# Optimization experiments

Hardware: AMD Instinct MI355X
Metric: run time of the kernel (lower is better)

The kernel has to match this reference:

```python
import jax, jax.numpy as jnp
import numpy as np

B, L, D, H, FF = 2, 4096, 512, 8, 2048
HD = D // H
EPS = 1e-5


def _layer_norm(x, g, b):
    mu = jnp.mean(x, axis=-1, keepdims=True)
    var = jnp.mean(jnp.square(x - mu), axis=-1, keepdims=True)
    return (x - mu) * jax.lax.rsqrt(var + EPS) * g + b


def setup_inputs() -> dict:
    key = jax.random.key(0)
    ks = jax.random.split(key, 16)
    s = 1.0 / np.sqrt(D)
    inp = {
        'x': jax.random.normal(ks[0], (B, L, D), dtype=jnp.float32),
        'Wq': jax.random.normal(ks[1], (D, D), dtype=jnp.float32) * s,
        'bq': jnp.zeros((D,), jnp.float32),
        'Wk': jax.random.normal(ks[2], (D, D), dtype=jnp.float32) * s,
        'bk': jnp.zeros((D,), jnp.float32),
        'Wv': jax.random.normal(ks[3], (D, D), dtype=jnp.float32) * s,
        'bv': jnp.zeros((D,), jnp.float32),
        'Wo': jax.random.normal(ks[4], (D, D), dtype=jnp.float32) * s,
        'bo': jnp.zeros((D,), jnp.float32),
        'ln1_g': jnp.ones((D,), jnp.float32),
        'ln1_b': jnp.zeros((D,), jnp.float32),
        'W1': jax.random.normal(ks[5], (D, FF), dtype=jnp.float32) * s,
        'b1': jnp.zeros((FF,), jnp.float32),
        'W2': jax.random.normal(ks[6], (FF, D), dtype=jnp.float32) * (1.0 / np.sqrt(FF)),
        'b2': jnp.zeros((D,), jnp.float32),
        'ln2_g': jnp.ones((D,), jnp.float32),
        'ln2_b': jnp.zeros((D,), jnp.float32),
        'window': 128,
    }
    return inp


def reference(x, Wq, bq, Wk, bk, Wv, bv, Wo, bo, ln1_g, ln1_b, W1, b1, W2, b2, ln2_g, ln2_b, window):
    # ---- local (banded) self-attention, matching nn.MultiheadAttention math ----
    q = (x @ Wq + bq).reshape(B, L, H, HD)
    k = (x @ Wk + bk).reshape(B, L, H, HD)
    v = (x @ Wv + bv).reshape(B, L, H, HD)
    scale = 1.0 / np.sqrt(HD)
    scores = jnp.einsum('bqhd,bkhd->bhqk', q, k) * scale  # [B,H,L,L]
    idx = jnp.arange(L)
    band = jnp.abs(idx[None, :] - idx[:, None]) > window   # True = masked
    scores = jnp.where(band[None, None], -jnp.inf, scores)
    probs = jax.nn.softmax(scores, axis=-1)
    attn = jnp.einsum('bhqk,bkhd->bqhd', probs, v).reshape(B, L, D)
    attn = attn @ Wo + bo
    # ---- residual + norm1 ----
    h = _layer_norm(x + attn, ln1_g, ln1_b)
    # ---- FFN + residual + norm2 (dropout=0 at eval) ----
    ff = jax.nn.relu(h @ W1 + b1) @ W2 + b2
    return _layer_norm(h + ff, ln2_g, ln2_b)
```

## Files before the change

kernel.cpp:

```cpp
#include <hip/hip_runtime.h>

namespace {

constexpr int B = 2, L = 4096, D = 512, H = 8, FF = 2048;
constexpr int M = B * L;
constexpr float LN_EPS = 1e-5f;

typedef __attribute__((ext_vector_type(8))) short short8;
typedef __attribute__((ext_vector_type(4))) float floatx4;

typedef __attribute__((address_space(3))) unsigned int lds_uint;
typedef const __attribute__((address_space(1))) unsigned int glob_uint;

__device__ __forceinline__ void gl_lds16(const unsigned short* g, unsigned short* l) {
  __builtin_amdgcn_global_load_lds((glob_uint*)g, (lds_uint*)l, 16, 0, 0);
}

__device__ __forceinline__ unsigned short f2bf(float f) {
  union { float f; unsigned u; } v; v.f = f;
  unsigned r = v.u + 0x7FFFu + ((v.u >> 16) & 1u);
  return (unsigned short)(r >> 16);
}

__device__ __forceinline__ float bf2f(unsigned short b) {
  union { unsigned u; float f; } v; v.u = ((unsigned)b) << 16;
  return v.f;
}

__global__ __launch_bounds__(256)
void k_prep(const float* __restrict__ x,
            const float* __restrict__ Wq, const float* __restrict__ Wk,
            const float* __restrict__ Wv, const float* __restrict__ Wo,
            const float* __restrict__ W1, const float* __restrict__ W2,
            const float* __restrict__ bq, const float* __restrict__ bk,
            const float* __restrict__ bv,
            unsigned short* __restrict__ Xb,
            unsigned short* __restrict__ WqkvT, unsigned short* __restrict__ WoT,
            unsigned short* __restrict__ W1T, unsigned short* __restrict__ W2T,
            float* __restrict__ bqkv) {
  __shared__ unsigned short tile[64 * 72];
  if (blockIdx.x < 4102) {
    int tid = blockIdx.x * blockDim.x + threadIdx.x;
    if (tid < 1048576) {
      float4 v = ((const float4*)x)[tid];
      ((ushort4*)Xb)[tid] = make_ushort4(f2bf(v.x), f2bf(v.y), f2bf(v.z), f2bf(v.w));
      return;
    }
    int u = tid - 1048576;
    if (u < 1536) bqkv[u] = (u < 512) ? bq[u] : (u < 1024 ? bk[u - 512] : bv[u - 1024]);
    return;
  }
  const int t = blockIdx.x - 4102;
  const float* src; unsigned short* dst; int Ns, Kd, n0, k0, nsrc0;
  if (t < 192) {
    int nt = t % 24, kt = t / 24; int ng = nt * 64;
    src = ng < 512 ? Wq : (ng < 1024 ? Wk : Wv);
    Ns = 512; Kd = 512; n0 = ng; nsrc0 = ng & 511; k0 = kt * 64; dst = WqkvT;
  } else if (t < 256) {
    int u = t - 192; int nt = u % 8, kt = u / 8;
    src = Wo; Ns = 512; Kd = 512; n0 = nt * 64; nsrc0 = n0; k0 = kt * 64; dst = WoT;
  } else if (t < 512) {
    int u = t - 256; int nt = u % 32, kt = u / 32;
    src = W1; Ns = 2048; Kd = 512; n0 = nt * 64; nsrc0 = n0; k0 = kt * 64; dst = W1T;
  } else {
    int u = t - 512; int nt = u % 8, kt = u / 8;
    src = W2; Ns = 512; Kd = 2048; n0 = nt * 64; nsrc0 = n0; k0 = kt * 64; dst = W2T;
  }
  const int tid = threadIdx.x;
  {
    int r = tid >> 2, cs = (tid & 3) * 16;
    const float4* sp = (const float4*)(src + (size_t)(k0 + r) * Ns + nsrc0 + cs);
    unsigned short* tp = &tile[r * 72 + cs];
#pragma unroll
    for (int i = 0; i < 4; ++i) {
      float4 v = sp[i];
      tp[i * 4 + 0] = f2bf(v.x); tp[i * 4 + 1] = f2bf(v.y);
      tp[i * 4 + 2] = f2bf(v.z); tp[i * 4 + 3] = f2bf(v.w);
    }
  }
  __syncthreads();
  {
    int n = tid >> 2, ks = (tid & 3) * 16;
    unsigned short buf[16];
#pragma unroll
    for (int e = 0; e < 16; ++e) buf[e] = tile[(ks + e) * 72 + n];
    unsigned short* dp = dst + (size_t)(n0 + n) * Kd + k0 + ks;
    *(short8*)dp = *(const short8*)&buf[0];
    *(short8*)(dp + 8) = *(const short8*)&buf[8];
  }
}

template <int EPI>
__global__ __launch_bounds__(256, 3)
void k_gemm(const unsigned short* __restrict__ A, const unsigned short* __restrict__ BT,
            const float* __restrict__ bias, void* __restrict__ Cout,
            unsigned short* __restrict__ Vout,
            const int klen, const int N) {
  __shared__ unsigned short lA[2][128 * 32];
  __shared__ unsigned short lB[2][128 * 32];
  unsigned flat = blockIdx.x + gridDim.x * (blockIdx.y + gridDim.y * blockIdx.z);
  const unsigned chunk = (gridDim.x * gridDim.y * gridDim.z) >> 3;
  flat = (flat & 7) * chunk + (flat >> 3);
  const unsigned bx = flat % gridDim.x;
  const unsigned rest = flat / gridDim.x;
  const unsigned by = rest % gridDim.y;
  const unsigned bz = rest / gridDim.y;

  const int tid = threadIdx.x;
  const int wave = tid >> 6, lane = tid & 63;
  const int quad = lane >> 4, l16 = lane & 15;
  const int m0 = by * 128, n0 = bx * 128;
  const int wm = (wave >> 1) * 64, wn = (wave & 1) * 64;
  const int kbeg = bz * klen;
  const size_t Kdim = (size_t)klen * gridDim.z;

  const floatx4 fzero = {0.f, 0.f, 0.f, 0.f};
  floatx4 acc[4][4];
#pragma unroll
  for (int i = 0; i < 4; ++i)
#pragma unroll
    for (int j = 0; j < 4; ++j) acc[i][j] = fzero;

  const int r0 = tid >> 2, o0 = (tid & 3) * 8;
  const int r1 = (256 + tid) >> 2, o1 = (tid & 3) * 8;
  const unsigned short* Ag0 = A + (size_t)(m0 + r0) * Kdim + kbeg + o0;
  const unsigned short* Ag1 = A + (size_t)(m0 + r1) * Kdim + kbeg + o1;
  const unsigned short* Bg0 = BT + (size_t)(n0 + r0) * Kdim + kbeg + o0;
  const unsigned short* Bg1 = BT + (size_t)(n0 + r1) * Kdim + kbeg + o1;

  auto stage = [&](int buf, int kt) {
    gl_lds16(Ag0 + kt, &lA[buf][wave * 512]);
    gl_lds16(Ag1 + kt, &lA[buf][(4 + wave) * 512]);
    gl_lds16(Bg0 + kt, &lB[buf][wave * 512]);
    gl_lds16(Bg1 + kt, &lB[buf][(4 + wave) * 512]);
  };

  stage(0, 0);
  __syncthreads();

  int buf = 0;
  for (int kt = 0; kt < klen; kt += 32, buf ^= 1) {
    if (kt + 32 < klen) stage(buf ^ 1, kt + 32);
    short8 af[4], bf[4];
#pragma unroll
    for (int i = 0; i < 4; ++i)
      af[i] = *(const short8*)&lA[buf][(wm + i * 16 + l16) * 32 + quad * 8];
#pragma unroll
    for (int j = 0; j < 4; ++j)
      bf[j] = *(const short8*)&lB[buf][(wn + j * 16 + l16) * 32 + quad * 8];
#pragma unroll
    for (int i = 0; i < 4; ++i)
#pragma unroll
      for (int j = 0; j < 4; ++j)
        acc[i][j] = __builtin_amdgcn_mfma_f32_16x16x32_bf16(af[i], bf[j], acc[i][j], 0, 0, 0);
    __syncthreads();
  }

  float* outf = (float*)Cout + (size_t)bz * M * N;
  const bool vblock = (EPI == 3) && (n0 >= 1024);
#pragma unroll
  for (int j = 0; j < 4; ++j) {
    const int col = n0 + wn + j * 16 + l16;
    const float bv = (bz == 0) ? bias[col] : 0.f;
#pragma unroll
    for (int i = 0; i < 4; ++i) {
      const int row = m0 + wm + i * 16 + quad * 4;
      if (EPI == 3 && vblock) {
        const int hh = (col - 1024) >> 6, dd = (col - 1024) & 63;
        const int bb = row >> 12, keyl = row & 4095;
        ushort4 pk = make_ushort4(f2bf(acc[i][j][0] + bv), f2bf(acc[i][j][1] + bv),
                                  f2bf(acc[i][j][2] + bv), f2bf(acc[i][j][3] + bv));
        *(ushort4*)(Vout + ((size_t)(bb * 8 + hh) * 64 + dd) * L + keyl) = pk;
      } else {
#pragma unroll
        for (int r = 0; r < 4; ++r) {
          float v = acc[i][j][r] + bv;
          if (EPI == 1) v = fmaxf(v, 0.f);
          if (EPI == 2)
            outf[(size_t)(row + r) * N + col] = v;
          else
            ((unsigned short*)Cout)[(size_t)(row + r) * N + col] = f2bf(v);
        }
      }
    }
  }
}

__global__ __launch_bounds__(256, 4)
void k_attn(const unsigned short* __restrict__ QKV, const unsigned short* __restrict__ Vg,
            unsigned short* __restrict__ attnb, const int* __restrict__ wptr) {
  const int W = wptr[0];
  __shared__ unsigned short Kt[2][4096];
  __shared__ unsigned short Vt[2][4096];
  const int tid = threadIdx.x;
  const int wave = tid >> 6, lane = tid & 63;
  const int quad = lane >> 4, l16 = lane & 15;
  const int bid = (int)((blockIdx.x & 7) * (gridDim.x >> 3) + (blockIdx.x >> 3));
  const int qt = bid & 63, h = (bid >> 6) & 7, b = bid >> 9;
  const int q0blk = qt * 64;
  const int q0 = q0blk + wave * 16;
  const float scale = 0.125f;

  const unsigned short* Kbase = QKV + (size_t)(b * L) * 1536 + 512 + h * 64;
  const unsigned short* Vh = Vg + (size_t)(b * 8 + h) * 64 * L;

  auto stage = [&](int buf, int jbg) {
#pragma unroll
    for (int i = 0; i < 2; ++i) {
      int c = i * 256 + tid;
      int kr = c >> 3;
      int key = jbg + kr;
      int keyc = key < 0 ? 0 : (key > L - 1 ? L - 1 : key);
      int dpart = (c & 7) ^ (kr & 7) ^ (((kr >> 3) & 3) << 1);
      gl_lds16(Kbase + (size_t)keyc * 1536 + dpart * 8,
               &Kt[buf][(i * 256 + wave * 64) * 8]);
    }
#pragma unroll
    for (int i = 0; i < 2; ++i) {
      int c = i * 256 + tid;
      int d = c >> 3;
      int kpart = (c & 7) ^ (d & 7);
      int kb = jbg + kpart * 8;
      kb = kb < 0 ? 0 : (kb > L - 8 ? L - 8 : kb);
      gl_lds16(Vh + (size_t)d * L + kb,
               &Vt[buf][(i * 256 + wave * 64) * 8]);
    }
  };

  const unsigned short* Qp = QKV + (size_t)(b * L + q0 + l16) * 1536 + h * 64;
  short8 qf0 = *(const short8*)(Qp + quad * 8);
  short8 qf1 = *(const short8*)(Qp + 32 + quad * 8);

  int koff[4][2];
#pragma unroll
  for (int tt = 0; tt < 4; ++tt) {
    int krow = (tt >> 1) * 32 + ((l16 >> 2) << 3) + (tt & 1) * 4 + (l16 & 3);
    int s2 = (krow & 7) ^ (((krow >> 3) & 3) << 1);
    koff[tt][0] = (krow * 8 + (quad ^ s2)) * 8;
    koff[tt][1] = (krow * 8 + ((quad + 4) ^ s2)) * 8;
  }
  int voff[4][2];
#pragma unroll
  for (int nt = 0; nt < 4; ++nt) {
    int d = nt * 16 + l16;
    voff[nt][0] = (d * 8 + (quad ^ (d & 7))) * 8;
    voff[nt][1] = (d * 8 + ((quad + 4) ^ (d & 7))) * 8;
  }

  const floatx4 fzero = {0.f, 0.f, 0.f, 0.f};
  floatx4 o[4];
#pragma unroll
  for (int i = 0; i < 4; ++i) o[i] = fzero;
  float lsum = 0.f;
  const int q = q0 + l16;

  stage(0, q0blk - 128);
  __syncthreads();

  for (int it = 0; it < 5; ++it) {
    const int jbg = q0blk - 128 + it * 64;
    if (it < 4) stage((it + 1) & 1, jbg + 64);
    const unsigned short* lk = Kt[it & 1];
    const unsigned short* lv = Vt[it & 1];
    const int dhi = q0 + 15 - jbg, dlo = jbg + 63 - q0;
    const bool fast = (jbg >= 0) && (jbg + 64 <= L) && ((dhi > dlo ? dhi : dlo) <= W);
    unsigned pu[8];
#pragma unroll
    for (int tt = 0; tt < 4; ++tt) {
      const short8 kf0 = *(const short8*)&lk[koff[tt][0]];
      const short8 kf1 = *(const short8*)&lk[koff[tt][1]];
      floatx4 z = fzero;
      z = __builtin_amdgcn_mfma_f32_16x16x32_bf16(kf0, qf0, z, 0, 0, 0);
      z = __builtin_amdgcn_mfma_f32_16x16x32_bf16(kf1, qf1, z, 0, 0, 0);
      float pv[4];
      if (fast) {
#pragma unroll
        for (int r = 0; r < 4; ++r) {
          float p = __expf(z[r] * scale);
          lsum += p;
          pv[r] = p;
        }
      } else {
        const int kb0 = jbg + (tt >> 1) * 32 + quad * 8 + (tt & 1) * 4;
#pragma unroll
        for (int r = 0; r < 4; ++r) {
          int key = kb0 + r;
          int dd = q - key; dd = dd < 0 ? -dd : dd;
          bool okk = (key >= 0) && (key < L) && (dd <= W);
          float p = okk ? __expf(z[r] * scale) : 0.f;
          lsum += p;
          pv[r] = p;
        }
      }
      unsigned lo, hi;
      asm("v_cvt_pk_bf16_f32 %0, %1, %2" : "=v"(lo) : "v"(pv[0]), "v"(pv[1]));
      asm("v_cvt_pk_bf16_f32 %0, %1, %2" : "=v"(hi) : "v"(pv[2]), "v"(pv[3]));
      pu[tt * 2 + 0] = lo;
      pu[tt * 2 + 1] = hi;
    }
    union { unsigned u[4]; short8 v; } pa0, pa1;
    pa0.u[0] = pu[0]; pa0.u[1] = pu[1]; pa0.u[2] = pu[2]; pa0.u[3] = pu[3];
    pa1.u[0] = pu[4]; pa1.u[1] = pu[5]; pa1.u[2] = pu[6]; pa1.u[3] = pu[7];
#pragma unroll
    for (int nt = 0; nt < 4; ++nt) {
      const short8 vf0 = *(const short8*)&lv[voff[nt][0]];
      const short8 vf1 = *(const short8*)&lv[voff[nt][1]];
      o[nt] = __builtin_amdgcn_mfma_f32_16x16x32_bf16(pa0.v, vf0, o[nt], 0, 0, 0);
      o[nt] = __builtin_amdgcn_mfma_f32_16x16x32_bf16(pa1.v, vf1, o[nt], 0, 0, 0);
    }
    __syncthreads();
  }
  lsum += __shfl_xor(lsum, 16, 64);
  lsum += __shfl_xor(lsum, 32, 64);
#pragma unroll
  for (int r = 0; r < 4; ++r) {
    float inv = 1.f / __shfl(lsum, quad * 4 + r, 64);
    size_t base = (size_t)(b * L + q0 + quad * 4 + r) * 512 + h * 64;
#pragma unroll
    for (int nt = 0; nt < 4; ++nt)
      attnb[base + nt * 16 + l16] = f2bf(o[nt][r] * inv);
  }
}

template <int RESBF>
__global__ __launch_bounds__(256, 2)
void k_res_ln(const float* __restrict__ t0, const float* __restrict__ t1,
              const void* __restrict__ res,
              const float* __restrict__ gamma, const float* __restrict__ beta,
              float* __restrict__ outf, unsigned short* __restrict__ outb) {
  const int wave = threadIdx.x >> 6, lane = threadIdx.x & 63;
  const int row = blockIdx.x * 4 + wave;
  const float4* tv = (const float4*)(t0 + (size_t)row * D);
  float4 a0 = tv[lane], a1 = tv[lane + 64];
  float4 b0, b1;
  if (RESBF) {
    const ushort4* rv = (const ushort4*)((const unsigned short*)res + (size_t)row * D);
    ushort4 u0 = rv[lane], u1 = rv[lane + 64];
    b0 = make_float4(bf2f(u0.x), bf2f(u0.y), bf2f(u0.z), bf2f(u0.w));
    b1 = make_float4(bf2f(u1.x), bf2f(u1.y), bf2f(u1.z), bf2f(u1.w));
  } else {
    const float4* rv = (const float4*)((const float*)res + (size_t)row * D);
    b0 = rv[lane]; b1 = rv[lane + 64];
  }
  float4 y0 = make_float4(a0.x + b0.x, a0.y + b0.y, a0.z + b0.z, a0.w + b0.w);
  float4 y1 = make_float4(a1.x + b1.x, a1.y + b1.y, a1.z + b1.z, a1.w + b1.w);
  {
    const float4* uv = (const float4*)(t1 + (size_t)row * D);
    float4 c0 = uv[lane], c1 = uv[lane + 64];
    y0.x += c0.x; y0.y += c0.y; y0.z += c0.z; y0.w += c0.w;
    y1.x += c1.x; y1.y += c1.y; y1.z += c1.z; y1.w += c1.w;
  }
  float s = y0.x + y0.y + y0.z + y0.w + y1.x + y1.y + y1.z + y1.w;
  float q = y0.x * y0.x + y0.y * y0.y + y0.z * y0.z + y0.w * y0.w +
            y1.x * y1.x + y1.y * y1.y + y1.z * y1.z + y1.w * y1.w;
#pragma unroll
  for (int d = 1; d < 64; d <<= 1) {
    s += __shfl_xor(s, d, 64);
    q += __shfl_xor(q, d, 64);
  }
  const float mean = s * (1.f / D);
  const float var = q * (1.f / D) - mean * mean;
  const float rstd = rsqrtf(var + LN_EPS);
  float4 g0 = ((const float4*)gamma)[lane], g1 = ((const float4*)gamma)[lane + 64];
  float4 e0 = ((const float4*)beta)[lane], e1 = ((const float4*)beta)[lane + 64];
  float4 o0 = make_float4((y0.x - mean) * rstd * g0.x + e0.x, (y0.y - mean) * rstd * g0.y + e0.y,
                          (y0.z - mean) * rstd * g0.z + e0.z, (y0.w - mean) * rstd * g0.w + e0.w);
  float4 o1 = make_float4((y1.x - mean) * rstd * g1.x + e1.x, (y1.y - mean) * rstd * g1.y + e1.y,
                          (y1.z - mean) * rstd * g1.z + e1.z, (y1.w - mean) * rstd * g1.w + e1.w);
  if (outf) {
    ((float4*)(outf + (size_t)row * D))[lane] = o0;
    ((float4*)(outf + (size_t)row * D))[lane + 64] = o1;
  }
  if (outb) {
    ((ushort4*)(outb + (size_t)row * D))[lane] =
        make_ushort4(f2bf(o0.x), f2bf(o0.y), f2bf(o0.z), f2bf(o0.w));
    ((ushort4*)(outb + (size_t)row * D))[lane + 64] =
        make_ushort4(f2bf(o1.x), f2bf(o1.y), f2bf(o1.z), f2bf(o1.w));
  }
}

}

extern "C" void kernel_launch(void* const* d_in, const int* in_sizes, int n_in,
                              void* d_out, int out_size, void* d_ws, size_t ws_size,
                              hipStream_t stream) {
  const float* x   = (const float*)d_in[0];
  const float* Wq  = (const float*)d_in[1];
  const float* bq  = (const float*)d_in[2];
  const float* Wk  = (const float*)d_in[3];
  const float* bk  = (const float*)d_in[4];
  const float* Wv  = (const float*)d_in[5];
  const float* bv  = (const float*)d_in[6];
  const float* Wo  = (const float*)d_in[7];
  const float* bo  = (const float*)d_in[8];
  const float* g1  = (const float*)d_in[9];
  const float* be1 = (const float*)d_in[10];
  const float* W1  = (const float*)d_in[11];
  const float* b1  = (const float*)d_in[12];
  const float* W2  = (const float*)d_in[13];
  const float* b2  = (const float*)d_in[14];
  const float* g2  = (const float*)d_in[15];
  const float* be2 = (const float*)d_in[16];
  const int* wptr  = (const int*)d_in[17];
  float* out = (float*)d_out;

  char* w = (char*)d_ws;
  size_t off = 0;
  auto take = [&](size_t bytes) -> void* {
    void* p = w + off;
    off += (bytes + 255) & ~(size_t)255;
    return p;
  };
  unsigned short* Xb    = (unsigned short*)take((size_t)M * D * 2);
  unsigned short* QKVb  = (unsigned short*)take((size_t)M * 1536 * 2);
  unsigned short* attnb = (unsigned short*)take((size_t)M * D * 2);
  unsigned short* Vg    = (unsigned short*)take((size_t)M * D * 2);
  unsigned short* WqkvT = (unsigned short*)take((size_t)1536 * 512 * 2);
  unsigned short* WoT   = (unsigned short*)take((size_t)512 * 512 * 2);
  unsigned short* W1T   = (unsigned short*)take((size_t)2048 * 512 * 2);
  unsigned short* W2T   = (unsigned short*)take((size_t)512 * 2048 * 2);
  float* bqkv           = (float*)take(1536 * 4);
  float* tbuf           = (float*)take((size_t)2 * M * D * 4);
  unsigned short* hb    = (unsigned short*)take((size_t)M * D * 2);
  unsigned short* ffb   = (unsigned short*)take((size_t)M * FF * 2);

  k_prep<<<4870, 256, 0, stream>>>(x, Wq, Wk, Wv, Wo, W1, W2, bq, bk, bv,
                                   Xb, WqkvT, WoT, W1T, W2T, bqkv);
  k_gemm<3><<<dim3(12, 64, 1), 256, 0, stream>>>(Xb, WqkvT, bqkv, QKVb, Vg, 512, 1536);
  k_attn<<<B * H * (L / 64), 256, 0, stream>>>(QKVb, Vg, attnb, wptr);
  k_gemm<2><<<dim3(4, 64, 2), 256, 0, stream>>>(attnb, WoT, bo, tbuf, nullptr, 256, 512);
  k_res_ln<0><<<M / 4, 256, 0, stream>>>(tbuf, tbuf + (size_t)M * D, x, g1, be1, nullptr, hb);
  k_gemm<1><<<dim3(16, 64, 1), 256, 0, stream>>>(hb, W1T, b1, ffb, nullptr, 512, 2048);
  k_gemm<2><<<dim3(4, 64, 2), 256, 0, stream>>>(ffb, W2T, b2, tbuf, nullptr, 1024, 512);
  k_res_ln<1><<<M / 4, 256, 0, stream>>>(tbuf, tbuf + (size_t)M * D, hb, g2, be2, out, nullptr);
}
```

Measured before the change: 233.7 us.

## Skip dead attention sub-tiles, fold Q scale into GEMM, drop Wo split-K

The attention softmax scale is now applied to Q in the QKV GEMM epilogue, which removes a multiply per score. The attention loop skips 32-key half tiles that lie completely outside the band or the sequence for a wave's 16 queries, saving their QK and PV MFMAs and LDS reads. The output-projection GEMM no longer uses a two-way split-K, so the layer-norm kernel reads a single partial buffer and skips the second load. The trade-offs are more branching in the attention inner loop and fewer blocks (less parallelism) for the Wo GEMM.

```diff
diff --git a/kernel.cpp b/kernel.cpp
--- a/kernel.cpp
+++ b/kernel.cpp
@@ -158,6 +158,7 @@
 
   float* outf = (float*)Cout + (size_t)bz * M * N;
   const bool vblock = (EPI == 3) && (n0 >= 1024);
+  const float qscale = (EPI == 3 && n0 < 512) ? 0.125f : 1.f;
 #pragma unroll
   for (int j = 0; j < 4; ++j) {
     const int col = n0 + wn + j * 16 + l16;
@@ -176,6 +177,7 @@
         for (int r = 0; r < 4; ++r) {
           float v = acc[i][j][r] + bv;
           if (EPI == 1) v = fmaxf(v, 0.f);
+          if (EPI == 3) v *= qscale;
           if (EPI == 2)
             outf[(size_t)(row + r) * N + col] = v;
           else
@@ -199,7 +201,6 @@
   const int qt = bid & 63, h = (bid >> 6) & 7, b = bid >> 9;
   const int q0blk = qt * 64;
   const int q0 = q0blk + wave * 16;
-  const float scale = 0.125f;
 
   const unsigned short* Kbase = QKV + (size_t)(b * L) * 1536 + 512 + h * 64;
   const unsigned short* Vh = Vg + (size_t)(b * 8 + h) * 64 * L;
@@ -262,11 +263,17 @@
     if (it < 4) stage((it + 1) & 1, jbg + 64);
     const unsigned short* lk = Kt[it & 1];
     const unsigned short* lv = Vt[it & 1];
-    const int dhi = q0 + 15 - jbg, dlo = jbg + 63 - q0;
-    const bool fast = (jbg >= 0) && (jbg + 64 <= L) && ((dhi > dlo ? dhi : dlo) <= W);
+    int lo = q0 - W - jbg;       if (-jbg > lo) lo = -jbg;
+    int hi = q0 + 15 + W - jbg;  if (L - 1 - jbg < hi) hi = L - 1 - jbg;
+    const bool alive0 = (hi >= 0) && (lo <= 31);
+    const bool alive1 = (hi >= 32) && (lo <= 63);
+    const bool fast = (jbg >= 0) && (jbg + 64 <= L) &&
+                      (q0 + 15 - jbg <= W) && (jbg + 63 - q0 <= W);
     unsigned pu[8];
+    union { unsigned u[4]; short8 v; } pa0, pa1;
 #pragma unroll
     for (int tt = 0; tt < 4; ++tt) {
+      if (tt < 2 ? !alive0 : !alive1) continue;
       const short8 kf0 = *(const short8*)&lk[koff[tt][0]];
       const short8 kf1 = *(const short8*)&lk[koff[tt][1]];
       floatx4 z = fzero;
@@ -276,7 +283,7 @@
       if (fast) {
 #pragma unroll
         for (int r = 0; r < 4; ++r) {
-          float p = __expf(z[r] * scale);
+          float p = __expf(z[r]);
           lsum += p;
           pv[r] = p;
         }
@@ -287,26 +294,31 @@
           int key = kb0 + r;
           int dd = q - key; dd = dd < 0 ? -dd : dd;
           bool okk = (key >= 0) && (key < L) && (dd <= W);
-          float p = okk ? __expf(z[r] * scale) : 0.f;
+          float p = okk ? __expf(z[r]) : 0.f;
           lsum += p;
           pv[r] = p;
         }
       }
-      unsigned lo, hi;
-      asm("v_cvt_pk_bf16_f32 %0, %1, %2" : "=v"(lo) : "v"(pv[0]), "v"(pv[1]));
-      asm("v_cvt_pk_bf16_f32 %0, %1, %2" : "=v"(hi) : "v"(pv[2]), "v"(pv[3]));
-      pu[tt * 2 + 0] = lo;
-      pu[tt * 2 + 1] = hi;
-    }
-    union { unsigned u[4]; short8 v; } pa0, pa1;
-    pa0.u[0] = pu[0]; pa0.u[1] = pu[1]; pa0.u[2] = pu[2]; pa0.u[3] = pu[3];
-    pa1.u[0] = pu[4]; pa1.u[1] = pu[5]; pa1.u[2] = pu[6]; pa1.u[3] = pu[7];
-#pragma unroll
-    for (int nt = 0; nt < 4; ++nt) {
-      const short8 vf0 = *(const short8*)&lv[voff[nt][0]];
-      const short8 vf1 = *(const short8*)&lv[voff[nt][1]];
-      o[nt] = __builtin_amdgcn_mfma_f32_16x16x32_bf16(pa0.v, vf0, o[nt], 0, 0, 0);
-      o[nt] = __builtin_amdgcn_mfma_f32_16x16x32_bf16(pa1.v, vf1, o[nt], 0, 0, 0);
+      unsigned lo2, hi2;
+      asm("v_cvt_pk_bf16_f32 %0, %1, %2" : "=v"(lo2) : "v"(pv[0]), "v"(pv[1]));
+      asm("v_cvt_pk_bf16_f32 %0, %1, %2" : "=v"(hi2) : "v"(pv[2]), "v"(pv[3]));
+      pu[tt * 2 + 0] = lo2;
+      pu[tt * 2 + 1] = hi2;
+    }
+    if (alive0) { pa0.u[0] = pu[0]; pa0.u[1] = pu[1]; pa0.u[2] = pu[2]; pa0.u[3] = pu[3]; }
+    if (alive1) { pa1.u[0] = pu[4]; pa1.u[1] = pu[5]; pa1.u[2] = pu[6]; pa1.u[3] = pu[7]; }
+    if (alive0 || alive1) {
+#pragma unroll
+      for (int nt = 0; nt < 4; ++nt) {
+        if (alive0) {
+          const short8 vf0 = *(const short8*)&lv[voff[nt][0]];
+          o[nt] = __builtin_amdgcn_mfma_f32_16x16x32_bf16(pa0.v, vf0, o[nt], 0, 0, 0);
+        }
+        if (alive1) {
+          const short8 vf1 = *(const short8*)&lv[voff[nt][1]];
+          o[nt] = __builtin_amdgcn_mfma_f32_16x16x32_bf16(pa1.v, vf1, o[nt], 0, 0, 0);
+        }
+      }
     }
     __syncthreads();
   }
@@ -344,7 +356,7 @@
   }
   float4 y0 = make_float4(a0.x + b0.x, a0.y + b0.y, a0.z + b0.z, a0.w + b0.w);
   float4 y1 = make_float4(a1.x + b1.x, a1.y + b1.y, a1.z + b1.z, a1.w + b1.w);
-  {
+  if (t1) {
     const float4* uv = (const float4*)(t1 + (size_t)row * D);
     float4 c0 = uv[lane], c1 = uv[lane + 64];
     y0.x += c0.x; y0.y += c0.y; y0.z += c0.z; y0.w += c0.w;
@@ -428,8 +440,8 @@
                                    Xb, WqkvT, WoT, W1T, W2T, bqkv);
   k_gemm<3><<<dim3(12, 64, 1), 256, 0, stream>>>(Xb, WqkvT, bqkv, QKVb, Vg, 512, 1536);
   k_attn<<<B * H * (L / 64), 256, 0, stream>>>(QKVb, Vg, attnb, wptr);
-  k_gemm<2><<<dim3(4, 64, 2), 256, 0, stream>>>(attnb, WoT, bo, tbuf, nullptr, 256, 512);
-  k_res_ln<0><<<M / 4, 256, 0, stream>>>(tbuf, tbuf + (size_t)M * D, x, g1, be1, nullptr, hb);
+  k_gemm<2><<<dim3(4, 64, 1), 256, 0, stream>>>(attnb, WoT, bo, tbuf, nullptr, 512, 512);
+  k_res_ln<0><<<M / 4, 256, 0, stream>>>(tbuf, nullptr, x, g1, be1, nullptr, hb);
   k_gemm<1><<<dim3(16, 64, 1), 256, 0, stream>>>(hb, W1T, b1, ffb, nullptr, 512, 2048);
   k_gemm<2><<<dim3(4, 64, 2), 256, 0, stream>>>(ffb, W2T, b2, tbuf, nullptr, 1024, 512);
   k_res_ln<1><<<M / 4, 256, 0, stream>>>(tbuf, tbuf + (size_t)M * D, hb, g2, be2, out, nullptr);
```

Result: slower. 258.7 us (+10.7%).
